# Optimization experiments

Measured on AMD Instinct MI355X. Metric: run time of the kernel, lower is better.

Reference implementation:

```python
import jax, jax.numpy as jnp
import numpy as np

B, S, C, E, H, D, V, K = 1024, 64, 512, 16, 1024, 256, 100, 2
NUM_NUM = 32  # num_numerical; categorical positions are S-NUM_NUM


def setup_inputs() -> dict:
    key = jax.random.key(0)
    ks = jax.random.split(key, 20)
    s = 0.02
    return {
        "codec": jax.random.normal(ks[0], (B, C), jnp.float32),
        "mask_pos": jax.random.randint(ks[1], (B, S), 0, 2, jnp.int32),
        "pos_emb": jax.random.normal(ks[2], (S, C), jnp.float32),
        "type_emb": jax.random.normal(ks[3], (2, C), jnp.float32),
        "gW1": jax.random.normal(ks[4], (3 * C + 1, 256), jnp.float32) * s,
        "gb1": jnp.zeros((256,), jnp.float32),
        "gW2": jax.random.normal(ks[5], (256, E), jnp.float32) * s,
        "gb2": jnp.zeros((E,), jnp.float32),
        "eW0": jax.random.normal(ks[6], (E, C, H), jnp.float32) * s,
        "eb0": jnp.zeros((E, H), jnp.float32),
        "eW1": jax.random.normal(ks[7], (E, H, H), jnp.float32) * s,
        "eb1": jnp.zeros((E, H), jnp.float32),
        "eW2": jax.random.normal(ks[8], (E, H, D), jnp.float32) * s,
        "eb2": jnp.zeros((E, D), jnp.float32),
        "nW": jax.random.normal(ks[9], (NUM_NUM, D), jnp.float32) * s,
        "nb": jnp.zeros((NUM_NUM,), jnp.float32),
        "cW": jax.random.normal(ks[10], (S - NUM_NUM, D, V), jnp.float32) * s,
        "cb": jnp.zeros((S - NUM_NUM, V), jnp.float32),
    }


def reference(codec, mask_pos, pos_emb, type_emb, gW1, gb1, gW2, gb2,
              eW0, eb0, eW1, eb1, eW2, eb2, nW, nb, cW, cb):
    maskf = mask_pos.astype(codec.dtype)  # [B,S]
    positions = jnp.arange(S)
    is_cat = (positions >= NUM_NUM).astype(jnp.int32)
    # gate input: [B,S,3C+1]
    gate_in = jnp.concatenate([
        jnp.broadcast_to(codec[:, None, :], (B, S, C)),
        jnp.broadcast_to(pos_emb[None], (B, S, C)),
        jnp.broadcast_to(type_emb[is_cat][None], (B, S, C)),
        maskf[..., None],
    ], axis=-1)
    h = jax.nn.gelu(gate_in @ gW1 + gb1, approximate=False)
    gate_logits = (h @ gW2 + gb2) * maskf[..., None]  # [B,S,E]
    topg, topi = jax.lax.top_k(gate_logits, K)  # [B,S,K]
    gates = jax.nn.softmax(topg, axis=-1)
    # all expert outputs on codec: [E,B,D]
    h0 = jax.nn.leaky_relu(jnp.einsum('bc,ech->ebh', codec, eW0) + eb0[:, None, :])
    h1 = jax.nn.leaky_relu(jnp.einsum('ebh,ehg->ebg', h0, eW1) + eb1[:, None, :])
    eout = jnp.einsum('ebg,egd->ebd', h1, eW2) + eb2[:, None, :]
    # per-token gather: tok[b,s,k,:] = eout[topi[b,s,k], b, :]
    eout_b = eout.transpose(1, 0, 2)  # [B,E,D]
    tok = jnp.take_along_axis(eout_b[:, None, :, :], topi[..., None], axis=2)  # [B,S,K,D]
    combined = jnp.einsum('bsk,bskd->bsd', gates, tok)  # [B,S,D]
    num_recon = jnp.einsum('bnd,nd->bn', combined[:, :NUM_NUM], nW) + nb  # [B,32]
    cat_recon = jnp.einsum('bnd,ndv->bnv', combined[:, NUM_NUM:], cW) + cb  # [B,32,V]
    return num_recon, cat_recon, gates, topi, mask_pos
```

## Files before the change

kernel.cpp:

```cpp
#include <hip/hip_runtime.h>
#include <hip/hip_bf16.h>

typedef __bf16 bf16x8 __attribute__((ext_vector_type(8)));
typedef float f32x4 __attribute__((ext_vector_type(4)));

static constexpr int B_ = 1024, S_ = 64, C_ = 512, E_ = 16, H_ = 1024, D_ = 256, V_ = 100;
static constexpr int NUMN = 32;

__device__ __forceinline__ unsigned short f2bf(float f) {
  union { float f; unsigned u; } x; x.f = f;
  unsigned r = x.u + 0x7fffu + ((x.u >> 16) & 1u);
  return (unsigned short)(r >> 16);
}

__device__ __forceinline__ float erf_fast(float x) {
  float ax = fabsf(x);
  float t = 1.0f / fmaf(0.3275911f, ax, 1.0f);
  float p = fmaf(1.061405429f, t, -1.453152027f);
  p = fmaf(p, t, 1.421413741f);
  p = fmaf(p, t, -0.284496736f);
  p = fmaf(p, t, 0.254829592f);
  p = p * t;
  float e = 1.0f - p * __expf(-ax * ax);
  return copysignf(e, x);
}

__global__ __launch_bounds__(256) void k_codec_bf(const float* __restrict__ src,
                                                  unsigned short* __restrict__ dst, int n) {
  int i = blockIdx.x * 256 + threadIdx.x;
  if (i < n) dst[i] = f2bf(src[i]);
}

__global__ __launch_bounds__(256) void k_transpose_bf(const float* __restrict__ W,
                                                      unsigned short* __restrict__ WT,
                                                      int K, int N) {
  __shared__ float t[32][33];
  int e = blockIdx.z;
  const float* We = W + (size_t)e * K * N;
  unsigned short* Te = WT + (size_t)e * N * K;
  int n0 = blockIdx.x * 32, k0 = blockIdx.y * 32;
  int tx = threadIdx.x & 31, ty = threadIdx.x >> 5;
#pragma unroll
  for (int i = 0; i < 32; i += 8) t[ty + i][tx] = We[(size_t)(k0 + ty + i) * N + n0 + tx];
  __syncthreads();
#pragma unroll
  for (int i = 0; i < 32; i += 8)
    Te[(size_t)(n0 + ty + i) * K + k0 + tx] = f2bf(t[tx][ty + i]);
}

__global__ __launch_bounds__(256) void k_cwt(const float* __restrict__ cW,
                                             unsigned short* __restrict__ cwt) {
  __shared__ float t[32][33];
  int n = blockIdx.z;
  const float* src = cW + (size_t)n * D_ * V_;
  unsigned short* dst = cwt + (size_t)n * 128 * 256;
  int v0 = blockIdx.x * 32, d0 = blockIdx.y * 32;
  int tx = threadIdx.x & 31, ty = threadIdx.x >> 5;
#pragma unroll
  for (int i = 0; i < 32; i += 8) {
    int v = v0 + tx;
    t[ty + i][tx] = (v < V_) ? src[(size_t)(d0 + ty + i) * V_ + v] : 0.f;
  }
  __syncthreads();
#pragma unroll
  for (int i = 0; i < 32; i += 8)
    dst[(size_t)(v0 + ty + i) * 256 + d0 + tx] = f2bf(t[tx][ty + i]);
}

__global__ __launch_bounds__(256) void k_cvt64(const float* __restrict__ gW2,
                                               const float* __restrict__ gW1,
                                               double* __restrict__ w2d,
                                               double* __restrict__ w1ld,
                                               int* __restrict__ flagcnt) {
  int i = blockIdx.x * 256 + threadIdx.x;
  if (i < 4096) w2d[i] = (double)gW2[i];
  if (i < 256) w1ld[i] = (double)gW1[(size_t)(3 * C_) * 256 + i];
  if (i == 0) *flagcnt = 0;
}

__global__ __launch_bounds__(256) void k_codecpart(const float* __restrict__ codec,
                                                   const float* __restrict__ gW1,
                                                   double* __restrict__ cp) {
  int j = threadIdx.x, b = blockIdx.x;
  const float* cb = codec + (size_t)b * C_;
  double a0 = 0, a1 = 0, a2 = 0, a3 = 0;
  for (int k = 0; k < C_; k += 4) {
    a0 += (double)cb[k] * (double)gW1[(size_t)k * 256 + j];
    a1 += (double)cb[k + 1] * (double)gW1[(size_t)(k + 1) * 256 + j];
    a2 += (double)cb[k + 2] * (double)gW1[(size_t)(k + 2) * 256 + j];
    a3 += (double)cb[k + 3] * (double)gW1[(size_t)(k + 3) * 256 + j];
  }
  cp[(size_t)b * 256 + j] = (a0 + a1) + (a2 + a3);
}

__global__ __launch_bounds__(256) void k_postype_part(const float* __restrict__ pos_emb,
                                                      const float* __restrict__ type_emb,
                                                      const float* __restrict__ gW1,
                                                      double* __restrict__ pp) {
  int j = threadIdx.x;
  int s = blockIdx.x;
  int kc = blockIdx.y;
  int tt = (s >= NUMN) ? 1 : 0;
  double a0 = 0, a1 = 0;
  int k0 = kc * 32;
  for (int kk = 0; kk < 32; kk += 2) {
    int k = k0 + kk;
    a0 += (double)pos_emb[(size_t)s * C_ + k] * (double)gW1[(size_t)(C_ + k) * 256 + j] +
          (double)type_emb[(size_t)tt * C_ + k] * (double)gW1[(size_t)(2 * C_ + k) * 256 + j];
    a1 += (double)pos_emb[(size_t)s * C_ + k + 1] * (double)gW1[(size_t)(C_ + k + 1) * 256 + j] +
          (double)type_emb[(size_t)tt * C_ + k + 1] * (double)gW1[(size_t)(2 * C_ + k + 1) * 256 + j];
  }
  pp[((size_t)kc * 64 + s) * 256 + j] = a0 + a1;
}

__global__ __launch_bounds__(256) void k_postype_red(const double* __restrict__ pp,
                                                     const float* __restrict__ gb1,
                                                     double* __restrict__ ptT) {
  int j = threadIdx.x;
  int s = blockIdx.x;
  double acc = (double)gb1[j];
#pragma unroll
  for (int kc = 0; kc < 16; ++kc) acc += pp[((size_t)kc * 64 + s) * 256 + j];
  ptT[(size_t)j * 64 + s] = acc;
}

__global__ __launch_bounds__(256) void k_gate(const double* __restrict__ cp,
                                              const double* __restrict__ ptT,
                                              const float* __restrict__ gW2,
                                              const double* __restrict__ w1ld,
                                              const float* __restrict__ gb2,
                                              const int* __restrict__ mask,
                                              float* __restrict__ out_g,
                                              float* __restrict__ out_i,
                                              float* __restrict__ out_m,
                                              float* __restrict__ tg,
                                              int* __restrict__ ti,
                                              int* __restrict__ flagcnt,
                                              int* __restrict__ flaglist) {
  __shared__ float red[3][64][17];
  int b = blockIdx.x;
  int s = threadIdx.x & 63;
  int wv = __builtin_amdgcn_readfirstlane(threadIdx.x >> 6);
  int token = b * 64 + s;
  double mf = (double)mask[token];
  const double* cpb = cp + (size_t)b * 256;
  float acc[16];
#pragma unroll
  for (int e = 0; e < 16; ++e) acc[e] = 0.f;
#pragma unroll 2
  for (int jj = 0; jj < 64; ++jj) {
    int j = wv * 64 + jj;
    double xd = cpb[j] + ptT[(size_t)j * 64 + s] + mf * w1ld[j];
    float x = (float)xd;
    float ef = erf_fast(x * 0.70710678f);
    float h = 0.5f * x * (1.0f + ef);
    const float* w2 = gW2 + (size_t)j * 16;
#pragma unroll
    for (int e = 0; e < 16; ++e) acc[e] = fmaf(h, w2[e], acc[e]);
  }
  if (wv > 0) {
#pragma unroll
    for (int e = 0; e < 16; ++e) red[wv - 1][s][e] = acc[e];
  }
  __syncthreads();
  if (wv == 0) {
    double vp[16];
#pragma unroll
    for (int e = 0; e < 16; ++e)
      vp[e] = (double)((acc[e] + red[0][s][e]) + (red[1][s][e] + red[2][s][e])) + (double)gb2[e];
    double margin;
    if (mf == 0.0) {
      double mn = 1e300;
#pragma unroll
      for (int e = 0; e < 16; ++e) mn = fmin(mn, fabs(vp[e]));
      margin = mn;
    } else {
      double t1 = -1e300, t2 = -1e300, t3 = -1e300;
#pragma unroll
      for (int e = 0; e < 16; ++e) {
        double v = vp[e];
        if (v > t1) { t3 = t2; t2 = t1; t1 = v; }
        else if (v > t2) { t3 = t2; t2 = v; }
        else if (v > t3) { t3 = v; }
      }
      margin = fmin(t1 - t2, t2 - t3);
    }
    if (margin < 1e-4) {
      int idx = atomicAdd(flagcnt, 1);
      if (idx < 8192) flaglist[idx] = token;
    }
    double v1, v2;
    int i1, i2;
    if (mf == 0.0) {
      int idx[2];
      int c = 0;
      for (int e = 0; e < 16 && c < 2; ++e)
        if (vp[e] > 0.0) idx[c++] = e;
      for (int e = 0; e < 16 && c < 2; ++e)
        if (!(vp[e] > 0.0)) idx[c++] = e;
      i1 = idx[0];
      i2 = idx[1];
      v1 = 0.0;
      v2 = 0.0;
    } else {
      v1 = -1e300; v2 = -1e300; i1 = 0; i2 = 1;
#pragma unroll
      for (int e = 0; e < 16; ++e) {
        double v = vp[e];
        if (v > v1) { v2 = v1; i2 = i1; v1 = v; i1 = e; }
        else if (v > v2) { v2 = v; i2 = e; }
      }
    }
    double ex = exp(v2 - v1);
    double den = 1.0 + ex;
    float g1 = (float)(1.0 / den), g2 = (float)(ex / den);
    out_g[(size_t)token * 2] = g1;
    out_g[(size_t)token * 2 + 1] = g2;
    out_i[(size_t)token * 2] = (float)i1;
    out_i[(size_t)token * 2 + 1] = (float)i2;
    out_m[token] = (float)mf;
    tg[(size_t)token * 2] = g1;
    tg[(size_t)token * 2 + 1] = g2;
    ti[(size_t)token * 2] = i1;
    ti[(size_t)token * 2 + 1] = i2;
  }
}

__global__ __launch_bounds__(64) void k_gate_fix(const double* __restrict__ cp,
                                                 const double* __restrict__ ptT,
                                                 const double* __restrict__ w2d,
                                                 const double* __restrict__ w1ld,
                                                 const float* __restrict__ gb2,
                                                 const int* __restrict__ mask,
                                                 const int* __restrict__ flagcnt,
                                                 const int* __restrict__ flaglist,
                                                 float* __restrict__ out_g,
                                                 float* __restrict__ out_i,
                                                 float* __restrict__ out_m,
                                                 float* __restrict__ tg,
                                                 int* __restrict__ ti) {
  int cnt = *flagcnt;
  if (cnt > 8192) cnt = 8192;
  int lane = threadIdx.x;
  for (int fi = blockIdx.x; fi < cnt; fi += gridDim.x) {
    int token = flaglist[fi];
    int b = token >> 6, sf = token & 63;
    double mf = (double)mask[token];
    const double* cpb = cp + (size_t)b * 256;
    double facc[16];
#pragma unroll
    for (int e = 0; e < 16; ++e) facc[e] = 0.0;
#pragma unroll
    for (int jj = 0; jj < 4; ++jj) {
      int j = jj * 64 + lane;
      double x = cpb[j] + ptT[(size_t)j * 64 + sf] + mf * w1ld[j];
      double h = 0.5 * x * (1.0 + erf(x * 0.70710678118654752440));
      const double* w2 = w2d + (size_t)j * 16;
#pragma unroll
      for (int e = 0; e < 16; ++e) facc[e] += h * w2[e];
    }
#pragma unroll
    for (int off = 32; off >= 1; off >>= 1) {
#pragma unroll
      for (int e = 0; e < 16; ++e) facc[e] += __shfl_xor(facc[e], off, 64);
    }
    if (lane == 0) {
      double vp[16];
#pragma unroll
      for (int e = 0; e < 16; ++e) vp[e] = facc[e] + (double)gb2[e];
      double v1, v2;
      int i1, i2;
      if (mf == 0.0) {
        int idx[2];
        int c = 0;
        for (int e = 0; e < 16 && c < 2; ++e)
          if (vp[e] > 0.0) idx[c++] = e;
        for (int e = 0; e < 16 && c < 2; ++e)
          if (!(vp[e] > 0.0)) idx[c++] = e;
        i1 = idx[0];
        i2 = idx[1];
        v1 = 0.0;
        v2 = 0.0;
      } else {
        v1 = -1e300; v2 = -1e300; i1 = 0; i2 = 1;
#pragma unroll
        for (int e = 0; e < 16; ++e) {
          double v = vp[e];
          if (v > v1) { v2 = v1; i2 = i1; v1 = v; i1 = e; }
          else if (v > v2) { v2 = v; i2 = e; }
        }
      }
      double ex = exp(v2 - v1);
      double den = 1.0 + ex;
      float g1 = (float)(1.0 / den), g2 = (float)(ex / den);
      out_g[(size_t)token * 2] = g1;
      out_g[(size_t)token * 2 + 1] = g2;
      out_i[(size_t)token * 2] = (float)i1;
      out_i[(size_t)token * 2 + 1] = (float)i2;
      out_m[token] = (float)mf;
      tg[(size_t)token * 2] = g1;
      tg[(size_t)token * 2 + 1] = g2;
      ti[(size_t)token * 2] = i1;
      ti[(size_t)token * 2 + 1] = i2;
    }
  }
}

__global__ __launch_bounds__(1024, 1) void k_gemm256(const unsigned short* __restrict__ A, size_t aStride,
                                                     const unsigned short* __restrict__ WT,
                                                     const float* __restrict__ bias,
                                                     unsigned short* __restrict__ Out,
                                                     int M, int N, int K) {
  extern __shared__ char lds[];
  char* sA = lds;
  char* sB = lds + 65536;
  int id = blockIdx.x + gridDim.x * (blockIdx.y + gridDim.y * blockIdx.z);
  int e = (id & 7) * 2 + ((id >> 3) & 1);
  int tile = id >> 4;
  int m0 = (tile & 3) * 256, n0 = (tile >> 2) * 256;
  const unsigned short* Ae = A + (size_t)e * aStride;
  const unsigned short* We = WT + (size_t)e * (size_t)N * K;
  int tid = threadIdx.x, lane = tid & 63, w = tid >> 6;
  int l15 = lane & 15, l4 = lane >> 4;
  int wr = (w >> 2) * 64;
  int wc = (w & 3) * 64;
  f32x4 acc[4][4] = {};
  int nk = K >> 6;

  auto stageA = [&](int buf, int h, int kt) {
    int off = tid * 16;
    int row = h * 128 + (off >> 7);
    int ss = ((off >> 4) & 7) ^ (row & 7);
    const char* src = (const char*)(Ae + (size_t)(m0 + row) * K + kt * 64) + ss * 16;
    __builtin_amdgcn_global_load_lds((const __attribute__((address_space(1))) void*)src,
        (__attribute__((address_space(3))) void*)(sA + buf * 32768 + h * 16384 + off), 16, 0, 0);
  };
  auto stageB = [&](int buf, int h, int kt) {
    int off = tid * 16;
    int row = h * 128 + (off >> 7);
    int ss = ((off >> 4) & 7) ^ (row & 7);
    const char* src = (const char*)(We + (size_t)(n0 + row) * K + kt * 64) + ss * 16;
    __builtin_amdgcn_global_load_lds((const __attribute__((address_space(1))) void*)src,
        (__attribute__((address_space(3))) void*)(sB + buf * 32768 + h * 16384 + off), 16, 0, 0);
  };
  auto ldA = [&](int buf, int mi, int ks) {
    int row = wr + mi * 16 + l15;
    int sp = (l4 + ks * 4) ^ (row & 7);
    return *(const bf16x8*)(sA + buf * 32768 + row * 128 + sp * 16);
  };
  auto ldB = [&](int buf, int ni, int ks) {
    int row = wc + ni * 16 + l15;
    int sp = (l4 + ks * 4) ^ (row & 7);
    return *(const bf16x8*)(sB + buf * 32768 + row * 128 + sp * 16);
  };

  stageA(0, 0, 0); stageA(0, 1, 0); stageB(0, 0, 0); stageB(0, 1, 0);
  asm volatile("s_waitcnt vmcnt(0)" ::: "memory");
  __builtin_amdgcn_s_barrier();

  for (int t = 0; t < nk; ++t) {
    int cur = t & 1, nxt = cur ^ 1;
    if (t + 1 < nk) {
      stageA(nxt, 0, t + 1); stageA(nxt, 1, t + 1);
      stageB(nxt, 0, t + 1); stageB(nxt, 1, t + 1);
    }
#pragma unroll
    for (int ks = 0; ks < 2; ++ks) {
      bf16x8 bfr[4], afr[4];
#pragma unroll
      for (int ni = 0; ni < 4; ++ni) bfr[ni] = ldB(cur, ni, ks);
#pragma unroll
      for (int mi = 0; mi < 4; ++mi) afr[mi] = ldA(cur, mi, ks);
      __builtin_amdgcn_s_setprio(1);
#pragma unroll
      for (int mi = 0; mi < 4; ++mi)
#pragma unroll
        for (int ni = 0; ni < 4; ++ni)
          acc[mi][ni] = __builtin_amdgcn_mfma_f32_16x16x32_bf16(afr[mi], bfr[ni], acc[mi][ni], 0, 0, 0);
      __builtin_amdgcn_s_setprio(0);
    }
    asm volatile("s_waitcnt vmcnt(0)" ::: "memory");
    __builtin_amdgcn_s_barrier();
  }

  size_t obase = (size_t)e * (size_t)M * N;
#pragma unroll
  for (int mi = 0; mi < 4; ++mi)
#pragma unroll
    for (int ni = 0; ni < 4; ++ni) {
      int col = n0 + wc + ni * 16 + l15;
      float bv = bias[(size_t)e * N + col];
#pragma unroll
      for (int j = 0; j < 4; ++j) {
        int row = m0 + wr + mi * 16 + l4 * 4 + j;
        float v = acc[mi][ni][j] + bv;
        v = (v > 0.f) ? v : 0.01f * v;
        Out[obase + (size_t)row * N + col] = f2bf(v);
      }
    }
}

template <int ACT, int OBF>
__global__ __launch_bounds__(256) void k_gemm(const unsigned short* __restrict__ A, size_t aStride,
                                              const unsigned short* __restrict__ WT,
                                              const float* __restrict__ bias,
                                              void* __restrict__ Out,
                                              int M, int N, int K) {
  __shared__ __align__(16) unsigned short sA[128 * 32];
  __shared__ __align__(16) unsigned short sB[128 * 32];
  int e = blockIdx.z;
  int m0 = blockIdx.x * 128, n0 = blockIdx.y * 128;
  const unsigned short* Ae = A + (size_t)e * aStride;
  const unsigned short* We = WT + (size_t)e * (size_t)N * K;
  int tid = threadIdx.x, lane = tid & 63, w = tid >> 6;
  int l15 = lane & 15, kh = (lane >> 4) * 8;
  int rsub = lane >> 2;
  int kk = (lane & 3) * 8;
  int wr = (w >> 1) * 64, wc = (w & 1) * 64;
  f32x4 acc[4][4] = {};
  int nk = K >> 5;

  auto stage = [&](int kt) {
#pragma unroll
    for (int c = 0; c < 2; ++c) {
      int chunk = w * 2 + c;
      int row = chunk * 16 + rsub;
      const unsigned short* ga = Ae + (size_t)(m0 + row) * K + kt * 32 + kk;
      __builtin_amdgcn_global_load_lds((const __attribute__((address_space(1))) void*)ga,
                                       (__attribute__((address_space(3))) void*)(&sA[chunk * 512]),
                                       16, 0, 0);
      const unsigned short* gb = We + (size_t)(n0 + row) * K + kt * 32 + kk;
      __builtin_amdgcn_global_load_lds((const __attribute__((address_space(1))) void*)gb,
                                       (__attribute__((address_space(3))) void*)(&sB[chunk * 512]),
                                       16, 0, 0);
    }
  };

  stage(0);
  for (int kt = 0; kt < nk; ++kt) {
    __syncthreads();
    bf16x8 a[4], bb[4];
#pragma unroll
    for (int mi = 0; mi < 4; ++mi)
      a[mi] = *(const bf16x8*)&sA[(wr + mi * 16 + l15) * 32 + kh];
#pragma unroll
    for (int ni = 0; ni < 4; ++ni)
      bb[ni] = *(const bf16x8*)&sB[(wc + ni * 16 + l15) * 32 + kh];
#pragma unroll
    for (int mi = 0; mi < 4; ++mi)
#pragma unroll
      for (int ni = 0; ni < 4; ++ni)
        acc[mi][ni] = __builtin_amdgcn_mfma_f32_16x16x32_bf16(a[mi], bb[ni], acc[mi][ni], 0, 0, 0);
    if (kt + 1 < nk) {
      __syncthreads();
      stage(kt + 1);
    }
  }

  unsigned short* outb = (unsigned short*)Out;
  float* outf = (float*)Out;
  size_t obase = (size_t)e * (size_t)M * N;
#pragma unroll
  for (int mi = 0; mi < 4; ++mi) {
#pragma unroll
    for (int ni = 0; ni < 4; ++ni) {
      int col = n0 + wc + ni * 16 + l15;
      float bv = bias[(size_t)e * N + col];
#pragma unroll
      for (int j = 0; j < 4; ++j) {
        int row = m0 + wr + mi * 16 + (lane >> 4) * 4 + j;
        float v = acc[mi][ni][j] + bv;
        if (ACT) v = (v > 0.f) ? v : 0.01f * v;
        if (OBF) outb[obase + (size_t)row * N + col] = f2bf(v);
        else outf[obase + (size_t)row * N + col] = v;
      }
    }
  }
}

__global__ __launch_bounds__(256) void k_comb(const float* __restrict__ eout,
                                              const float* __restrict__ tg,
                                              const int* __restrict__ ti,
                                              unsigned short* __restrict__ combbf) {
  int b = blockIdx.x, n = blockIdx.y, d = threadIdx.x;
  int tk = b * 64 + 32 + n;
  float g1 = tg[(size_t)tk * 2], g2 = tg[(size_t)tk * 2 + 1];
  int i1 = ti[(size_t)tk * 2], i2 = ti[(size_t)tk * 2 + 1];
  float v = g1 * eout[((size_t)i1 * B_ + b) * D_ + d] + g2 * eout[((size_t)i2 * B_ + b) * D_ + d];
  combbf[((size_t)n * B_ + b) * D_ + d] = f2bf(v);
}

__global__ __launch_bounds__(256) void k_catgemm(const unsigned short* __restrict__ combbf,
                                                 const unsigned short* __restrict__ cwt,
                                                 const float* __restrict__ cb,
                                                 float* __restrict__ out1) {
  __shared__ __align__(16) unsigned short sA[128 * 32];
  __shared__ __align__(16) unsigned short sB[128 * 32];
  int n = blockIdx.z;
  int m0 = blockIdx.x * 128;
  const unsigned short* Ae = combbf + (size_t)n * B_ * D_;
  const unsigned short* We = cwt + (size_t)n * 128 * 256;
  int tid = threadIdx.x, lane = tid & 63, w = tid >> 6;
  int l15 = lane & 15, kh = (lane >> 4) * 8;
  int rsub = lane >> 2;
  int kk = (lane & 3) * 8;
  int wr = (w >> 1) * 64, wc = (w & 1) * 64;
  f32x4 acc[4][4] = {};
  const int K = 256, nk = K >> 5;

  auto stage = [&](int kt) {
#pragma unroll
    for (int c = 0; c < 2; ++c) {
      int chunk = w * 2 + c;
      int row = chunk * 16 + rsub;
      const unsigned short* ga = Ae + (size_t)(m0 + row) * K + kt * 32 + kk;
      __builtin_amdgcn_global_load_lds((const __attribute__((address_space(1))) void*)ga,
                                       (__attribute__((address_space(3))) void*)(&sA[chunk * 512]),
                                       16, 0, 0);
      const unsigned short* gb = We + (size_t)row * K + kt * 32 + kk;
      __builtin_amdgcn_global_load_lds((const __attribute__((address_space(1))) void*)gb,
                                       (__attribute__((address_space(3))) void*)(&sB[chunk * 512]),
                                       16, 0, 0);
    }
  };

  stage(0);
  for (int kt = 0; kt < nk; ++kt) {
    __syncthreads();
    bf16x8 a[4], bb[4];
#pragma unroll
    for (int mi = 0; mi < 4; ++mi)
      a[mi] = *(const bf16x8*)&sA[(wr + mi * 16 + l15) * 32 + kh];
#pragma unroll
    for (int ni = 0; ni < 4; ++ni)
      bb[ni] = *(const bf16x8*)&sB[(wc + ni * 16 + l15) * 32 + kh];
#pragma unroll
    for (int mi = 0; mi < 4; ++mi)
#pragma unroll
      for (int ni = 0; ni < 4; ++ni)
        acc[mi][ni] = __builtin_amdgcn_mfma_f32_16x16x32_bf16(a[mi], bb[ni], acc[mi][ni], 0, 0, 0);
    if (kt + 1 < nk) {
      __syncthreads();
      stage(kt + 1);
    }
  }

#pragma unroll
  for (int mi = 0; mi < 4; ++mi) {
#pragma unroll
    for (int ni = 0; ni < 4; ++ni) {
      int col = wc + ni * 16 + l15;
      if (col < V_) {
        float bv = cb[(size_t)n * V_ + col];
#pragma unroll
        for (int j = 0; j < 4; ++j) {
          int row = m0 + wr + mi * 16 + (lane >> 4) * 4 + j;
          out1[((size_t)row * 32 + n) * V_ + col] = acc[mi][ni][j] + bv;
        }
      }
    }
  }
}

__global__ __launch_bounds__(256) void k_num(const float* __restrict__ eout,
                                             const float* __restrict__ nW,
                                             const float* __restrict__ nb,
                                             const float* __restrict__ tg,
                                             const int* __restrict__ ti,
                                             float* __restrict__ out0) {
  int b = blockIdx.x;
  int lane = threadIdx.x & 63;
  int wv = threadIdx.x >> 6;
#pragma unroll
  for (int q = 0; q < 8; ++q) {
    int n = wv * 8 + q;
    int tk = b * 64 + n;
    float g1 = tg[(size_t)tk * 2], g2 = tg[(size_t)tk * 2 + 1];
    int i1 = ti[(size_t)tk * 2], i2 = ti[(size_t)tk * 2 + 1];
    const float4* p1 = (const float4*)(eout + ((size_t)i1 * B_ + b) * D_);
    const float4* p2 = (const float4*)(eout + ((size_t)i2 * B_ + b) * D_);
    const float4* wp = (const float4*)(nW + (size_t)n * D_);
    float4 a = p1[lane], c = p2[lane], ww = wp[lane];
    float acc = fmaf(g1, a.x, g2 * c.x) * ww.x + fmaf(g1, a.y, g2 * c.y) * ww.y +
                fmaf(g1, a.z, g2 * c.z) * ww.z + fmaf(g1, a.w, g2 * c.w) * ww.w;
#pragma unroll
    for (int off = 32; off >= 1; off >>= 1) acc += __shfl_xor(acc, off, 64);
    if (lane == 0) out0[(size_t)b * 32 + n] = nb[n] + acc;
  }
}

extern "C" void kernel_launch(void* const* d_in, const int* in_sizes, int n_in,
                              void* d_out, int out_size, void* d_ws, size_t ws_size,
                              hipStream_t stream) {
  const float* codec = (const float*)d_in[0];
  const int* maskp = (const int*)d_in[1];
  const float* pos_emb = (const float*)d_in[2];
  const float* type_emb = (const float*)d_in[3];
  const float* gW1 = (const float*)d_in[4];
  const float* gb1 = (const float*)d_in[5];
  const float* gW2 = (const float*)d_in[6];
  const float* gb2 = (const float*)d_in[7];
  const float* eW0 = (const float*)d_in[8];
  const float* eb0 = (const float*)d_in[9];
  const float* eW1 = (const float*)d_in[10];
  const float* eb1 = (const float*)d_in[11];
  const float* eW2 = (const float*)d_in[12];
  const float* eb2 = (const float*)d_in[13];
  const float* nW = (const float*)d_in[14];
  const float* nb = (const float*)d_in[15];
  const float* cW = (const float*)d_in[16];
  const float* cb = (const float*)d_in[17];

  char* ws = (char*)d_ws;
  size_t o = 0;
  unsigned short* codecbf = (unsigned short*)(ws + o); o += (size_t)B_ * C_ * 2;
  size_t o_w0t = o;
  unsigned short* w0t = (unsigned short*)(ws + o); o += (size_t)E_ * H_ * C_ * 2;
  unsigned short* w1t = (unsigned short*)(ws + o); o += (size_t)E_ * H_ * H_ * 2;
  unsigned short* w2t = (unsigned short*)(ws + o); o += (size_t)E_ * D_ * H_ * 2;
  size_t o_h0 = o;
  unsigned short* h0 = (unsigned short*)(ws + o); o += (size_t)E_ * B_ * H_ * 2;
  unsigned short* h1 = (unsigned short*)(ws + o); o += (size_t)E_ * B_ * H_ * 2;
  double* cp = (double*)(ws + o); o += (size_t)B_ * 256 * 8;
  double* ptT = (double*)(ws + o); o += (size_t)S_ * 256 * 8;
  float* tg = (float*)(ws + o); o += (size_t)B_ * S_ * 2 * 4;
  int* ti = (int*)(ws + o); o += (size_t)B_ * S_ * 2 * 4;
  double* w2d = (double*)(ws + o); o += 4096 * 8;
  double* w1ld = (double*)(ws + o); o += 256 * 8;
  unsigned short* cwt = (unsigned short*)(ws + o); o += (size_t)32 * 128 * 256 * 2;
  double* pp = (double*)(ws + o); o += (size_t)16 * 64 * 256 * 8;
  int* flagcnt = (int*)(ws + o); o += 256;
  int* flaglist = (int*)(ws + o); o += 8192 * 4;
  float* eout = (float*)(ws + o_w0t);
  unsigned short* combbf = (unsigned short*)(ws + o_h0);

  float* out = (float*)d_out;
  float* out_num = out;
  float* out_cat = out + 32768;
  float* out_g = out + 32768 + 3276800;
  float* out_i = out_g + (size_t)B_ * S_ * 2;
  float* out_m = out_i + (size_t)B_ * S_ * 2;

  hipLaunchKernelGGL(k_codec_bf, dim3((B_ * C_) / 256), dim3(256), 0, stream, codec, codecbf, B_ * C_);
  hipLaunchKernelGGL(k_cvt64, dim3(16), dim3(256), 0, stream, gW2, gW1, w2d, w1ld, flagcnt);
  hipLaunchKernelGGL(k_transpose_bf, dim3(H_ / 32, C_ / 32, E_), dim3(256), 0, stream, eW0, w0t, C_, H_);
  hipLaunchKernelGGL(k_transpose_bf, dim3(H_ / 32, H_ / 32, E_), dim3(256), 0, stream, eW1, w1t, H_, H_);
  hipLaunchKernelGGL(k_transpose_bf, dim3(D_ / 32, H_ / 32, E_), dim3(256), 0, stream, eW2, w2t, H_, D_);
  hipLaunchKernelGGL(k_cwt, dim3(4, 8, 32), dim3(256), 0, stream, cW, cwt);
  hipLaunchKernelGGL(k_codecpart, dim3(B_), dim3(256), 0, stream, codec, gW1, cp);
  hipLaunchKernelGGL(k_postype_part, dim3(S_, 16), dim3(256), 0, stream, pos_emb, type_emb, gW1, pp);
  hipLaunchKernelGGL(k_postype_red, dim3(S_), dim3(256), 0, stream, pp, gb1, ptT);
  hipLaunchKernelGGL(k_gate, dim3(B_), dim3(256), 0, stream, cp, ptT, gW2, w1ld, gb2,
                     maskp, out_g, out_i, out_m, tg, ti, flagcnt, flaglist);
  hipLaunchKernelGGL(k_gate_fix, dim3(2048), dim3(64), 0, stream, cp, ptT, w2d, w1ld, gb2,
                     maskp, flagcnt, flaglist, out_g, out_i, out_m, tg, ti);
  hipLaunchKernelGGL(k_gemm256, dim3(4, 4, E_), dim3(1024), 131072, stream,
                     codecbf, (size_t)0, w0t, eb0, h0, 1024, 1024, 512);
  hipLaunchKernelGGL(k_gemm256, dim3(4, 4, E_), dim3(1024), 131072, stream,
                     h0, (size_t)(B_ * H_), w1t, eb1, h1, 1024, 1024, 1024);
  hipLaunchKernelGGL((k_gemm<0, 0>), dim3(8, 2, E_), dim3(256), 0, stream,
                     h1, (size_t)(B_ * H_), w2t, eb2, (void*)eout, 1024, 256, 1024);
  hipLaunchKernelGGL(k_comb, dim3(B_, 32), dim3(256), 0, stream, eout, tg, ti, combbf);
  hipLaunchKernelGGL(k_num, dim3(B_), dim3(256), 0, stream, eout, nW, nb, tg, ti, out_num);
  hipLaunchKernelGGL(k_catgemm, dim3(8, 1, 32), dim3(256), 0, stream, combbf, cwt, cb, out_cat);
}
```

Measured before the change: 233.8 us.

## Fuse expert-combine gather into categorical GEMM A-tile staging with double buffering

Removes the separate k_comb kernel that wrote gate-weighted bf16 combined activations to global memory. k_catgemm now gathers the two selected expert outputs per row, applies the gates, converts to bf16 and writes directly into shared memory. It also double-buffers the A and B shared tiles so the next tile loads while the current MFMAs run. This saves one launch and a round trip through global memory, but the A staging now uses synchronous scalar fp32 loads instead of async global-to-LDS copies.

```diff
diff --git a/kernel.cpp b/kernel.cpp
--- a/kernel.cpp
+++ b/kernel.cpp
@@ -478,27 +478,16 @@
   }
 }
 
-__global__ __launch_bounds__(256) void k_comb(const float* __restrict__ eout,
-                                              const float* __restrict__ tg,
-                                              const int* __restrict__ ti,
-                                              unsigned short* __restrict__ combbf) {
-  int b = blockIdx.x, n = blockIdx.y, d = threadIdx.x;
-  int tk = b * 64 + 32 + n;
-  float g1 = tg[(size_t)tk * 2], g2 = tg[(size_t)tk * 2 + 1];
-  int i1 = ti[(size_t)tk * 2], i2 = ti[(size_t)tk * 2 + 1];
-  float v = g1 * eout[((size_t)i1 * B_ + b) * D_ + d] + g2 * eout[((size_t)i2 * B_ + b) * D_ + d];
-  combbf[((size_t)n * B_ + b) * D_ + d] = f2bf(v);
-}
-
-__global__ __launch_bounds__(256) void k_catgemm(const unsigned short* __restrict__ combbf,
+__global__ __launch_bounds__(256) void k_catgemm(const float* __restrict__ eout,
                                                  const unsigned short* __restrict__ cwt,
                                                  const float* __restrict__ cb,
+                                                 const float* __restrict__ tg,
+                                                 const int* __restrict__ ti,
                                                  float* __restrict__ out1) {
-  __shared__ __align__(16) unsigned short sA[128 * 32];
-  __shared__ __align__(16) unsigned short sB[128 * 32];
+  __shared__ __align__(16) unsigned short sA[2][128 * 32];
+  __shared__ __align__(16) unsigned short sB[2][128 * 32];
   int n = blockIdx.z;
   int m0 = blockIdx.x * 128;
-  const unsigned short* Ae = combbf + (size_t)n * B_ * D_;
   const unsigned short* We = cwt + (size_t)n * 128 * 256;
   int tid = threadIdx.x, lane = tid & 63, w = tid >> 6;
   int l15 = lane & 15, kh = (lane >> 4) * 8;
@@ -508,41 +497,66 @@
   f32x4 acc[4][4] = {};
   const int K = 256, nk = K >> 5;
 
-  auto stage = [&](int kt) {
+  float g1v[2], g2v[2];
+  const float* p1v[2];
+  const float* p2v[2];
+#pragma unroll
+  for (int c = 0; c < 2; ++c) {
+    int row = (w * 2 + c) * 16 + rsub;
+    int bb = m0 + row;
+    int tk = bb * 64 + 32 + n;
+    g1v[c] = tg[(size_t)tk * 2];
+    g2v[c] = tg[(size_t)tk * 2 + 1];
+    int i1 = ti[(size_t)tk * 2], i2 = ti[(size_t)tk * 2 + 1];
+    p1v[c] = eout + ((size_t)i1 * B_ + bb) * D_;
+    p2v[c] = eout + ((size_t)i2 * B_ + bb) * D_;
+  }
+
+  auto stageA = [&](int buf, int kt) {
+#pragma unroll
+    for (int c = 0; c < 2; ++c) {
+      int row = (w * 2 + c) * 16 + rsub;
+      const float* q1 = p1v[c] + kt * 32 + kk;
+      const float* q2 = p2v[c] + kt * 32 + kk;
+      unsigned short vals[8];
+#pragma unroll
+      for (int k = 0; k < 8; ++k) vals[k] = f2bf(g1v[c] * q1[k] + g2v[c] * q2[k]);
+      *(uint4*)&sA[buf][row * 32 + kk] = *(uint4*)vals;
+    }
+  };
+  auto stageB = [&](int buf, int kt) {
 #pragma unroll
     for (int c = 0; c < 2; ++c) {
       int chunk = w * 2 + c;
       int row = chunk * 16 + rsub;
-      const unsigned short* ga = Ae + (size_t)(m0 + row) * K + kt * 32 + kk;
-      __builtin_amdgcn_global_load_lds((const __attribute__((address_space(1))) void*)ga,
-                                       (__attribute__((address_space(3))) void*)(&sA[chunk * 512]),
-                                       16, 0, 0);
       const unsigned short* gb = We + (size_t)row * K + kt * 32 + kk;
       __builtin_amdgcn_global_load_lds((const __attribute__((address_space(1))) void*)gb,
-                                       (__attribute__((address_space(3))) void*)(&sB[chunk * 512]),
+                                       (__attribute__((address_space(3))) void*)(&sB[buf][chunk * 512]),
                                        16, 0, 0);
     }
   };
 
-  stage(0);
+  stageA(0, 0);
+  stageB(0, 0);
   for (int kt = 0; kt < nk; ++kt) {
+    int cur = kt & 1;
     __syncthreads();
+    if (kt + 1 < nk) {
+      stageA(cur ^ 1, kt + 1);
+      stageB(cur ^ 1, kt + 1);
+    }
     bf16x8 a[4], bb[4];
 #pragma unroll
     for (int mi = 0; mi < 4; ++mi)
-      a[mi] = *(const bf16x8*)&sA[(wr + mi * 16 + l15) * 32 + kh];
+      a[mi] = *(const bf16x8*)&sA[cur][(wr + mi * 16 + l15) * 32 + kh];
 #pragma unroll
     for (int ni = 0; ni < 4; ++ni)
-      bb[ni] = *(const bf16x8*)&sB[(wc + ni * 16 + l15) * 32 + kh];
+      bb[ni] = *(const bf16x8*)&sB[cur][(wc + ni * 16 + l15) * 32 + kh];
 #pragma unroll
     for (int mi = 0; mi < 4; ++mi)
 #pragma unroll
       for (int ni = 0; ni < 4; ++ni)
         acc[mi][ni] = __builtin_amdgcn_mfma_f32_16x16x32_bf16(a[mi], bb[ni], acc[mi][ni], 0, 0, 0);
-    if (kt + 1 < nk) {
-      __syncthreads();
-      stage(kt + 1);
-    }
   }
 
 #pragma unroll
@@ -632,7 +646,7 @@
   int* flagcnt = (int*)(ws + o); o += 256;
   int* flaglist = (int*)(ws + o); o += 8192 * 4;
   float* eout = (float*)(ws + o_w0t);
-  unsigned short* combbf = (unsigned short*)(ws + o_h0);
+  (void)o_h0;
 
   float* out = (float*)d_out;
   float* out_num = out;
@@ -660,7 +674,6 @@
                      h0, (size_t)(B_ * H_), w1t, eb1, h1, 1024, 1024, 1024);
   hipLaunchKernelGGL((k_gemm<0, 0>), dim3(8, 2, E_), dim3(256), 0, stream,
                      h1, (size_t)(B_ * H_), w2t, eb2, (void*)eout, 1024, 256, 1024);
-  hipLaunchKernelGGL(k_comb, dim3(B_, 32), dim3(256), 0, stream, eout, tg, ti, combbf);
   hipLaunchKernelGGL(k_num, dim3(B_), dim3(256), 0, stream, eout, nW, nb, tg, ti, out_num);
-  hipLaunchKernelGGL(k_catgemm, dim3(8, 1, 32), dim3(256), 0, stream, combbf, cwt, cb, out_cat);
-}
+  hipLaunchKernelGGL(k_catgemm, dim3(8, 1, 32), dim3(256), 0, stream, eout, cwt, cb, tg, ti, out_cat);
+}
```

After: 223.8 us. 1.04x faster.
